# Kernel tuning notes

Measured on AMD Instinct MI355X. Metric: run time of the kernel, lower is better.

The kernel has to match this reference:

```python
import jax, jax.numpy as jnp
import numpy as np
from jax import lax

A = 20            # len(ANCHOR_RATIOS)=4 * len(ANCHOR_SCALES)=5 in neural-motifs config
TGT = 6           # anchor_target_dim
DIM = 512
IN_DIM = 1024
B, H, W = 16, 37, 37


def setup_inputs() -> dict:
    key = jax.random.key(0)
    k1, k2, k3, k4, k5 = jax.random.split(key, 5)
    fmap = jax.random.normal(k1, (B, IN_DIM, H, W), dtype=jnp.float32)
    # conv weights in OIHW, fan-in scaled init
    W1 = jax.random.normal(k2, (DIM, IN_DIM, 3, 3), dtype=jnp.float32) / np.sqrt(IN_DIM * 9)
    b1 = jnp.zeros((DIM,), dtype=jnp.float32)
    W2 = jax.random.normal(k3, (TGT * A, DIM, 1, 1), dtype=jnp.float32) / np.sqrt(DIM)
    b2 = jnp.zeros((TGT * A,), dtype=jnp.float32)
    return {"fmap": fmap, "W1": W1, "b1": b1, "W2": W2, "b2": b2}


def reference(fmap, W1, b1, W2, b2):
    dn = ("NCHW", "OIHW", "NCHW")
    # 3x3 conv, padding=1
    x = lax.conv_general_dilated(fmap, W1, window_strides=(1, 1), padding="SAME",
                                 dimension_numbers=dn) + b1[None, :, None, None]
    # ReLU6
    x = jnp.clip(x, 0.0, 6.0)
    # 1x1 conv -> [B, 6*A, H, W]
    x = lax.conv_general_dilated(x, W2, window_strides=(1, 1), padding="VALID",
                                 dimension_numbers=dn) + b2[None, :, None, None]
    # _reshape_channels: [B, C, H, W] -> [B, H, W, C], then split C -> (A, 6)
    b, c, h, w = x.shape
    x = jnp.transpose(x, (0, 2, 3, 1))
    return x.reshape(b, h, w, A, TGT)
```

## Files before the change

### kernel.cpp

```cpp
#include <hip/hip_runtime.h>
#include <stdint.h>

#define HW   1369
#define QW   39
#define QP   1616
#define QT   1536
#define CIN  1024
#define CMID 512
#define KTOT 9216
#define NTIL 144
#define ASL  12288

typedef float  f32x4  __attribute__((ext_vector_type(4)));
typedef __bf16 bf16x8 __attribute__((ext_vector_type(8)));

__device__ __forceinline__ uint16_t f2bf(float f) {
  uint32_t u = __float_as_uint(f);
  u += 0x7fffu + ((u >> 16) & 1u);
  return (uint16_t)(u >> 16);
}

__device__ __forceinline__ void gll16(const void* g, void* l) {
  const __attribute__((address_space(1))) uint32_t* ga =
      (const __attribute__((address_space(1))) uint32_t*)(uintptr_t)g;
  __attribute__((address_space(3))) uint32_t* la =
      (__attribute__((address_space(3))) uint32_t*)(uint32_t)(uintptr_t)l;
  __builtin_amdgcn_global_load_lds(ga, la, 16, 0, 0);
}

__global__ void k_pad_transpose(const float* __restrict__ fmap, uint16_t* __restrict__ Xp) {
  __shared__ float t[32][33];
  const int b = blockIdx.z;
  const int c0 = blockIdx.y * 32;
  const int p0 = blockIdx.x * 32;
  const int tx = threadIdx.x, ty = threadIdx.y;
  const float* src = fmap + ((size_t)b * CIN + c0) * HW + p0;
#pragma unroll
  for (int i = 0; i < 4; ++i) {
    int cc = ty + i * 8;
    t[cc][tx] = (p0 + tx < HW) ? src[(size_t)cc * HW + tx] : 0.f;
  }
  __syncthreads();
#pragma unroll
  for (int i = 0; i < 4; ++i) {
    int pl = ty + i * 8;
    int p = p0 + pl;
    if (p < HW) {
      int h = p / 37, w = p - h * 37;
      int q = (h + 1) * QW + (w + 1);
      Xp[((size_t)b * QP + q) * CIN + c0 + tx] = f2bf(t[tx][pl]);
    }
  }
}

__global__ void k_pack_bfrag(const float* __restrict__ W1, uint16_t* __restrict__ Bp) {
  const int gid = blockIdx.x * 256 + threadIdx.x;
  const int lane = gid & 63;
  const int f    = gid >> 6;
  const int kk   = f & 1;
  const int o16  = (f >> 1) & 31;
  const int t    = f >> 6;
  const int cb = t / 9, tap = t - cb * 9;
  const int o   = o16 * 16 + (lane & 15);
  const int kap = kk * 32 + (lane >> 4) * 8;
  uint16_t* dst = Bp + (size_t)gid * 8;
#pragma unroll
  for (int e = 0; e < 8; ++e) {
    const int c = cb * 64 + kap + e;
    dst[e] = f2bf(W1[((size_t)o * CIN + c) * 9 + tap]);
  }
}

__global__ void k_pack_w2(const float* __restrict__ W2, uint16_t* __restrict__ W2p) {
  int idx = blockIdx.x * 256 + threadIdx.x;
  int j = idx >> 9, o = idx & 511;
  W2p[idx] = (j < 120) ? f2bf(W2[j * 512 + o]) : (uint16_t)0;
}

__global__ __launch_bounds__(256, 2) void k_conv1(
    const uint16_t* __restrict__ Xp, const uint16_t* __restrict__ Bp,
    const float* __restrict__ b1, uint16_t* __restrict__ x1) {
  __shared__ __align__(16) uint16_t lds[2 * ASL];

  const int tid  = threadIdx.x;
  const int wid  = tid >> 6, lane = tid & 63;
  const int lrow = lane & 15, lq = lane >> 4;
  const int wm   = wid >> 1,  wn = wid & 1;

  const int bid = blockIdx.x;
  const int g   = (bid & 7) * 64 + (bid >> 3);
  const int mt  = g >> 2, nt = g & 3;
  const int batch = mt >> 3, qb = (mt & 7) * 192;
  const int o0 = nt * 128;
  const uint16_t* Xb = Xp + (size_t)batch * QP * CIN;

  const int xorb    = (lrow & 7) << 4;
  const int col_el0 = ((lq * 16) ^ xorb) >> 1;
  const int col_el1 = col_el0 ^ 32;

  const int scol = ((tid & 7) ^ ((tid >> 3) & 7)) * 8;
  const int srow = tid >> 3;

  const uint16_t* Bpl = Bp + (size_t)lane * 8;
  const int o16b = nt * 8 + wn * 4;

  f32x4 acc[6][4] = {};

#define STAGEA(u) do {                                                                \
    if ((u) < NTIL) {                                                                 \
      const int cb_  = (u) / 9;                                                       \
      const int tap_ = (u) - cb_ * 9;                                                 \
      const int off_ = (tap_ / 3) * QW + tap_ % 3;                                    \
      const int c0_  = cb_ << 6;                                                      \
      uint16_t* sa = lds + ((u) & 1) * ASL;                                           \
      _Pragma("unroll")                                                               \
      for (int j = 0; j < 6; ++j)                                                     \
        gll16(Xb + (size_t)(qb + off_ + j * 32 + srow) * CIN + c0_ + scol,            \
              sa + (j * 256 + wid * 64) * 8);                                         \
    }                                                                                 \
  } while (0)

#define LOADB(u, BV) do {                                                             \
    if ((u) < NTIL) {                                                                 \
      _Pragma("unroll")                                                               \
      for (int n = 0; n < 4; ++n)                                                     \
        _Pragma("unroll")                                                             \
        for (int kk = 0; kk < 2; ++kk)                                                \
          BV[n * 2 + kk] = *(const bf16x8*)(                                          \
              Bpl + (((size_t)(u) * 32 + o16b + n) * 2 + kk) * 512);                  \
    }                                                                                 \
  } while (0)

#define TILE(t, BVC, BVN) do {                                                        \
    const uint16_t* As = lds + ((t) & 1) * ASL;                                       \
    asm volatile("s_waitcnt vmcnt(0)" ::: "memory");   \
    asm volatile("s_barrier" ::: "memory");                                           \
    __builtin_amdgcn_sched_barrier(0);                                                \
    STAGEA((t) + 1);                                                                  \
    LOADB((t) + 1, BVN);                                                              \
    bf16x8 av0[6], av1[6];                                                            \
    _Pragma("unroll")                                                                 \
    for (int m = 0; m < 6; ++m) {                                                     \
      const uint16_t* ar = As + (wm * 96 + m * 16 + lrow) * 64;                       \
      av0[m] = *(const bf16x8*)(ar + col_el0);                                        \
      av1[m] = *(const bf16x8*)(ar + col_el1);                                        \
    }                                                                                 \
    __builtin_amdgcn_s_setprio(1);                                                    \
    _Pragma("unroll")                                                                 \
    for (int m = 0; m < 6; ++m)                                                       \
      _Pragma("unroll")                                                               \
      for (int n = 0; n < 4; ++n)                                                     \
        acc[m][n] = __builtin_amdgcn_mfma_f32_16x16x32_bf16(                          \
            av0[m], BVC[n * 2], acc[m][n], 0, 0, 0);                                  \
    _Pragma("unroll")                                                                 \
    for (int m = 0; m < 6; ++m)                                                       \
      _Pragma("unroll")                                                               \
      for (int n = 0; n < 4; ++n)                                                     \
        acc[m][n] = __builtin_amdgcn_mfma_f32_16x16x32_bf16(                          \
            av1[m], BVC[n * 2 + 1], acc[m][n], 0, 0, 0);                              \
    __builtin_amdgcn_s_setprio(0);                                                    \
  } while (0)

  bf16x8 bvX[8], bvY[8];
  LOADB(0, bvX);
  STAGEA(0);

  for (int t = 0; t < NTIL; t += 2) {
    TILE(t,     bvX, bvY);
    TILE(t + 1, bvY, bvX);
  }

  const int qr = lq * 4;
#pragma unroll
  for (int n = 0; n < 4; ++n) {
    const int o = o0 + wn * 64 + n * 16 + lrow;
    const float bias = b1[o];
#pragma unroll
    for (int m = 0; m < 6; ++m) {
#pragma unroll
      for (int v = 0; v < 4; ++v) {
        const int q = qb + wm * 96 + m * 16 + qr + v;
        float x = acc[m][n][v] + bias;
        x = fminf(fmaxf(x, 0.f), 6.f);
        x1[((size_t)batch * QT + q) * CMID + o] = f2bf(x);
      }
    }
  }
#undef TILE
#undef LOADB
#undef STAGEA
}

__global__ __launch_bounds__(256, 2) void k_conv2(
    const uint16_t* __restrict__ x1, const uint16_t* __restrict__ W2p,
    const float* __restrict__ b2, float* __restrict__ out) {
  __shared__ __align__(16) uint16_t lA[128 * 64];
  __shared__ __align__(16) uint16_t lB[128 * 64];
  const int tid = threadIdx.x;
  const int wid = tid >> 6, lane = tid & 63;
  const int b = blockIdx.z, q0 = blockIdx.x * 128;
  const uint16_t* Ab = x1 + (size_t)b * QT * CMID;
  const int wm = wid >> 1, wn = wid & 1;
  const int lrow = lane & 15, lk = (lane >> 4) * 8;
  f32x4 acc[4][4] = {};

  for (int kt = 0; kt < 8; ++kt) {
    const int c0 = kt << 6;
#pragma unroll
    for (int i = 0; i < 4; ++i) {
      int wb = i * 256 + wid * 64;
      int chunk = wb + lane;
      int row = chunk >> 3, ch = chunk & 7;
      gll16(Ab + (size_t)(q0 + row) * CMID + c0 + ch * 8, lA + wb * 8);
      gll16(W2p + (size_t)row * CMID + c0 + ch * 8, lB + wb * 8);
    }
    __syncthreads();
#pragma unroll
    for (int kk = 0; kk < 2; ++kk) {
      bf16x8 av[4], bv[4];
#pragma unroll
      for (int mi = 0; mi < 4; ++mi)
        av[mi] = *(const bf16x8*)(lA + (wm * 64 + mi * 16 + lrow) * 64 + kk * 32 + lk);
#pragma unroll
      for (int ni = 0; ni < 4; ++ni)
        bv[ni] = *(const bf16x8*)(lB + (wn * 64 + ni * 16 + lrow) * 64 + kk * 32 + lk);
#pragma unroll
      for (int mi = 0; mi < 4; ++mi)
#pragma unroll
        for (int ni = 0; ni < 4; ++ni)
          acc[mi][ni] = __builtin_amdgcn_mfma_f32_16x16x32_bf16(av[mi], bv[ni], acc[mi][ni], 0, 0, 0);
    }
    __syncthreads();
  }

  const int qr = (lane >> 4) * 4;
#pragma unroll
  for (int ni = 0; ni < 4; ++ni) {
    int j = wn * 64 + ni * 16 + lrow;
    if (j < 120) {
      float bias = b2[j];
#pragma unroll
      for (int mi = 0; mi < 4; ++mi) {
#pragma unroll
        for (int v = 0; v < 4; ++v) {
          int q = q0 + wm * 64 + mi * 16 + qr + v;
          int h = q / QW, w = q - h * QW;
          if (h < 37 && w < 37) {
            out[((size_t)b * HW + h * 37 + w) * 120 + j] = acc[mi][ni][v] + bias;
          }
        }
      }
    }
  }
}

extern "C" void kernel_launch(void* const* d_in, const int* in_sizes, int n_in,
                              void* d_out, int out_size, void* d_ws, size_t ws_size,
                              hipStream_t stream) {
  const float* fmap = (const float*)d_in[0];
  const float* W1   = (const float*)d_in[1];
  const float* b1   = (const float*)d_in[2];
  const float* W2   = (const float*)d_in[3];
  const float* b2   = (const float*)d_in[4];
  float* out = (float*)d_out;

  uint8_t* ws = (uint8_t*)d_ws;
  const size_t XP_BYTES = (size_t)16 * QP * CIN * 2;
  const size_t BP_BYTES = (size_t)144 * 32 * 2 * 64 * 8 * 2;
  const size_t W2P_BYTES = (size_t)128 * 512 * 2;
  uint16_t* Xp  = (uint16_t*)ws;
  uint16_t* Bp  = (uint16_t*)(ws + XP_BYTES);
  uint16_t* W2p = (uint16_t*)(ws + XP_BYTES + BP_BYTES);
  uint16_t* x1  = (uint16_t*)(ws + XP_BYTES + BP_BYTES + W2P_BYTES);

  hipMemsetAsync(Xp, 0, XP_BYTES, stream);
  k_pad_transpose<<<dim3(43, 32, 16), dim3(32, 8), 0, stream>>>(fmap, Xp);
  k_pack_bfrag<<<dim3(2304), dim3(256), 0, stream>>>(W1, Bp);
  k_pack_w2<<<dim3(256), dim3(256), 0, stream>>>(W2, W2p);
  k_conv1<<<dim3(512), dim3(256), 0, stream>>>(Xp, Bp, b1, x1);
  k_conv2<<<dim3(12, 1, 16), dim3(256), 0, stream>>>(x1, W2p, b2, out);
}
```

Measured before the change: 260.1 us.

## Give each wave a private A slice in conv1 and drop block barriers

The conv1 GEMM is repartitioned so each wave owns 48 output rows across all 128 output channels. Each wave stages its own A rows into a private LDS region, which removes the block-wide s_barrier. B fragments are now fetched with inline-asm global loads split by k-half, and explicit vmcnt waits overlap the next tile's loads with the current MFMAs. The trade-off is that every wave must load all 128 channels of B per tile, roughly doubling B global traffic. It also depends on hand-counted vmcnt values, which can silently break correctness if the number of in-flight loads changes.

```diff
diff --git a/kernel.cpp b/kernel.cpp
--- a/kernel.cpp
+++ b/kernel.cpp
@@ -9,7 +9,6 @@
 #define CMID 512
 #define KTOT 9216
 #define NTIL 144
-#define ASL  12288
 
 typedef float  f32x4  __attribute__((ext_vector_type(4)));
 typedef __bf16 bf16x8 __attribute__((ext_vector_type(8)));
@@ -80,12 +79,11 @@
 __global__ __launch_bounds__(256, 2) void k_conv1(
     const uint16_t* __restrict__ Xp, const uint16_t* __restrict__ Bp,
     const float* __restrict__ b1, uint16_t* __restrict__ x1) {
-  __shared__ __align__(16) uint16_t lds[2 * ASL];
+  __shared__ __align__(16) uint16_t lds[24576];
 
   const int tid  = threadIdx.x;
   const int wid  = tid >> 6, lane = tid & 63;
   const int lrow = lane & 15, lq = lane >> 4;
-  const int wm   = wid >> 1,  wn = wid & 1;
 
   const int bid = blockIdx.x;
   const int g   = (bid & 7) * 64 + (bid >> 3);
@@ -93,18 +91,21 @@
   const int batch = mt >> 3, qb = (mt & 7) * 192;
   const int o0 = nt * 128;
   const uint16_t* Xb = Xp + (size_t)batch * QP * CIN;
+  const int qw = qb + wid * 48;
+
+  const int srow8 = lane >> 3;
+  const int scol  = ((lane & 7) ^ srow8) * 8;
+
+  uint16_t* myl = lds + wid * 6144;
 
   const int xorb    = (lrow & 7) << 4;
   const int col_el0 = ((lq * 16) ^ xorb) >> 1;
   const int col_el1 = col_el0 ^ 32;
 
-  const int scol = ((tid & 7) ^ ((tid >> 3) & 7)) * 8;
-  const int srow = tid >> 3;
-
-  const uint16_t* Bpl = Bp + (size_t)lane * 8;
-  const int o16b = nt * 8 + wn * 4;
-
-  f32x4 acc[6][4] = {};
+  const uint16_t* Bl = Bp + (size_t)lane * 8 + (size_t)nt * 8192;
+
+  f32x4 acc[3][8] = {};
+  bf16x8 bv0[8], bv1[8];
 
 #define STAGEA(u) do {                                                                \
     if ((u) < NTIL) {                                                                 \
@@ -112,74 +113,78 @@
       const int tap_ = (u) - cb_ * 9;                                                 \
       const int off_ = (tap_ / 3) * QW + tap_ % 3;                                    \
       const int c0_  = cb_ << 6;                                                      \
-      uint16_t* sa = lds + ((u) & 1) * ASL;                                           \
+      uint16_t* sl = myl + ((u) & 1) * 3072;                                          \
       _Pragma("unroll")                                                               \
       for (int j = 0; j < 6; ++j)                                                     \
-        gll16(Xb + (size_t)(qb + off_ + j * 32 + srow) * CIN + c0_ + scol,            \
-              sa + (j * 256 + wid * 64) * 8);                                         \
+        gll16(Xb + (size_t)(qw + off_ + j * 8 + srow8) * CIN + c0_ + scol,            \
+              sl + j * 512);                                                          \
     }                                                                                 \
   } while (0)
 
-#define LOADB(u, BV) do {                                                             \
+#define LOADBK(u, kk, BV) do {                                                        \
     if ((u) < NTIL) {                                                                 \
-      _Pragma("unroll")                                                               \
-      for (int n = 0; n < 4; ++n)                                                     \
-        _Pragma("unroll")                                                             \
-        for (int kk = 0; kk < 2; ++kk)                                                \
-          BV[n * 2 + kk] = *(const bf16x8*)(                                          \
-              Bpl + (((size_t)(u) * 32 + o16b + n) * 2 + kk) * 512);                  \
+      const uint16_t* bq = Bl + ((size_t)(u) * 64 + (kk)) * 512;                      \
+      _Pragma("unroll")                                                               \
+      for (int n = 0; n < 8; ++n)                                                     \
+        asm volatile("global_load_dwordx4 %0, %1, off"                                \
+                     : "=v"(BV[n]) : "v"(bq + n * 1024) : "memory");                  \
     }                                                                                 \
   } while (0)
 
-#define TILE(t, BVC, BVN) do {                                                        \
-    const uint16_t* As = lds + ((t) & 1) * ASL;                                       \
-    asm volatile("s_waitcnt vmcnt(0)" ::: "memory");   \
-    asm volatile("s_barrier" ::: "memory");                                           \
+#define TILE(t, W1S, W2S, ISS) do {                                                   \
+    asm volatile(W1S ::: "memory");                          \
     __builtin_amdgcn_sched_barrier(0);                                                \
-    STAGEA((t) + 1);                                                                  \
-    LOADB((t) + 1, BVN);                                                              \
-    bf16x8 av0[6], av1[6];                                                            \
+    const uint16_t* As = myl + ((t) & 1) * 3072;                                      \
+    bf16x8 av0[3], av1[3];                                                            \
     _Pragma("unroll")                                                                 \
-    for (int m = 0; m < 6; ++m) {                                                     \
-      const uint16_t* ar = As + (wm * 96 + m * 16 + lrow) * 64;                       \
+    for (int m = 0; m < 3; ++m) {                                                     \
+      const uint16_t* ar = As + (m * 16 + lrow) * 64;                                 \
       av0[m] = *(const bf16x8*)(ar + col_el0);                                        \
       av1[m] = *(const bf16x8*)(ar + col_el1);                                        \
     }                                                                                 \
     __builtin_amdgcn_s_setprio(1);                                                    \
     _Pragma("unroll")                                                                 \
-    for (int m = 0; m < 6; ++m)                                                       \
-      _Pragma("unroll")                                                               \
-      for (int n = 0; n < 4; ++n)                                                     \
+    for (int m = 0; m < 3; ++m)                                                       \
+      _Pragma("unroll")                                                               \
+      for (int n = 0; n < 8; ++n)                                                     \
         acc[m][n] = __builtin_amdgcn_mfma_f32_16x16x32_bf16(                          \
-            av0[m], BVC[n * 2], acc[m][n], 0, 0, 0);                                  \
+            av0[m], bv0[n], acc[m][n], 0, 0, 0);                                      \
+    __builtin_amdgcn_s_setprio(0);                                                    \
+    if (ISS) { LOADBK((t) + 1, 0, bv0); STAGEA((t) + 1); }                            \
+    asm volatile(W2S ::: "memory");                                 \
+    __builtin_amdgcn_sched_barrier(0);                                                \
+    __builtin_amdgcn_s_setprio(1);                                                    \
     _Pragma("unroll")                                                                 \
-    for (int m = 0; m < 6; ++m)                                                       \
-      _Pragma("unroll")                                                               \
-      for (int n = 0; n < 4; ++n)                                                     \
+    for (int m = 0; m < 3; ++m)                                                       \
+      _Pragma("unroll")                                                               \
+      for (int n = 0; n < 8; ++n)                                                     \
         acc[m][n] = __builtin_amdgcn_mfma_f32_16x16x32_bf16(                          \
-            av1[m], BVC[n * 2 + 1], acc[m][n], 0, 0, 0);                              \
+            av1[m], bv1[n], acc[m][n], 0, 0, 0);                                      \
     __builtin_amdgcn_s_setprio(0);                                                    \
+    if (ISS) LOADBK((t) + 1, 1, bv1);                                                 \
   } while (0)
 
-  bf16x8 bvX[8], bvY[8];
-  LOADB(0, bvX);
+  LOADBK(0, 0, bv0);
   STAGEA(0);
-
-  for (int t = 0; t < NTIL; t += 2) {
-    TILE(t,     bvX, bvY);
-    TILE(t + 1, bvY, bvX);
-  }
+  LOADBK(0, 1, bv1);
+
+  for (int t = 0; t < NTIL - 2; t += 2) {
+    TILE(t,     "s_waitcnt vmcnt(8)",  "s_waitcnt vmcnt(14)", 1);
+    TILE(t + 1, "s_waitcnt vmcnt(8)",  "s_waitcnt vmcnt(14)", 1);
+  }
+  TILE(NTIL - 2, "s_waitcnt vmcnt(8)", "s_waitcnt vmcnt(14)", 1);
+  TILE(NTIL - 1, "s_waitcnt vmcnt(8)", "s_waitcnt vmcnt(0)",  0);
 
   const int qr = lq * 4;
 #pragma unroll
-  for (int n = 0; n < 4; ++n) {
-    const int o = o0 + wn * 64 + n * 16 + lrow;
+  for (int n = 0; n < 8; ++n) {
+    const int o = o0 + n * 16 + lrow;
     const float bias = b1[o];
 #pragma unroll
-    for (int m = 0; m < 6; ++m) {
+    for (int m = 0; m < 3; ++m) {
 #pragma unroll
       for (int v = 0; v < 4; ++v) {
-        const int q = qb + wm * 96 + m * 16 + qr + v;
+        const int q = qw + m * 16 + qr + v;
         float x = acc[m][n][v] + bias;
         x = fminf(fmaxf(x, 0.f), 6.f);
         x1[((size_t)batch * QT + q) * CMID + o] = f2bf(x);
@@ -187,7 +192,7 @@
     }
   }
 #undef TILE
-#undef LOADB
+#undef LOADBK
 #undef STAGEA
 }
 
```

New measurement: 297.5 us. 14.4% more time.

## Stage one halo panel per channel block and reuse it across all nine taps

Applied to the files above, without the earlier changes.

The conv1 implicit GEMM used to stage a separate shifted A tile from global memory for each of the 144 (channel-block, tap) steps. It now loads one 288-row halo panel per 64-channel block into LDS and reads all nine tap offsets from that panel. The swizzle is rebased on the tap row offset so the XOR pattern still matches. This cuts global-to-LDS traffic about ninefold and needs only one barrier per channel block instead of one per tap. In exchange LDS use grows to 72 KB per block, which may limit occupancy at two blocks per CU, and the padded input buffer is enlarged to cover the panel overrun.

```diff
diff --git a/kernel.cpp b/kernel.cpp
--- a/kernel.cpp
+++ b/kernel.cpp
@@ -3,13 +3,12 @@
 
 #define HW   1369
 #define QW   39
-#define QP   1616
+#define QP2  1648
 #define QT   1536
 #define CIN  1024
 #define CMID 512
-#define KTOT 9216
 #define NTIL 144
-#define ASL  12288
+#define PANEL 18432
 
 typedef float  f32x4  __attribute__((ext_vector_type(4)));
 typedef __bf16 bf16x8 __attribute__((ext_vector_type(8)));
@@ -48,7 +47,7 @@
     if (p < HW) {
       int h = p / 37, w = p - h * 37;
       int q = (h + 1) * QW + (w + 1);
-      Xp[((size_t)b * QP + q) * CIN + c0 + tx] = f2bf(t[tx][pl]);
+      Xp[((size_t)b * QP2 + q) * CIN + c0 + tx] = f2bf(t[tx][pl]);
     }
   }
 }
@@ -80,7 +79,7 @@
 __global__ __launch_bounds__(256, 2) void k_conv1(
     const uint16_t* __restrict__ Xp, const uint16_t* __restrict__ Bp,
     const float* __restrict__ b1, uint16_t* __restrict__ x1) {
-  __shared__ __align__(16) uint16_t lds[2 * ASL];
+  __shared__ __align__(16) uint16_t lds[2 * PANEL];
 
   const int tid  = threadIdx.x;
   const int wid  = tid >> 6, lane = tid & 63;
@@ -92,31 +91,23 @@
   const int mt  = g >> 2, nt = g & 3;
   const int batch = mt >> 3, qb = (mt & 7) * 192;
   const int o0 = nt * 128;
-  const uint16_t* Xb = Xp + (size_t)batch * QP * CIN;
-
-  const int xorb    = (lrow & 7) << 4;
-  const int col_el0 = ((lq * 16) ^ xorb) >> 1;
-  const int col_el1 = col_el0 ^ 32;
-
-  const int scol = ((tid & 7) ^ ((tid >> 3) & 7)) * 8;
-  const int srow = tid >> 3;
+  const uint16_t* Xb = Xp + (size_t)batch * QP2 * CIN;
+
+  const int sR8  = lane >> 3;
+  const int sc8  = ((lane & 7) ^ sR8) * 8;
 
   const uint16_t* Bpl = Bp + (size_t)lane * 8;
   const int o16b = nt * 8 + wn * 4;
 
   f32x4 acc[6][4] = {};
-
-#define STAGEA(u) do {                                                                \
-    if ((u) < NTIL) {                                                                 \
-      const int cb_  = (u) / 9;                                                       \
-      const int tap_ = (u) - cb_ * 9;                                                 \
-      const int off_ = (tap_ / 3) * QW + tap_ % 3;                                    \
-      const int c0_  = cb_ << 6;                                                      \
-      uint16_t* sa = lds + ((u) & 1) * ASL;                                           \
-      _Pragma("unroll")                                                               \
-      for (int j = 0; j < 6; ++j)                                                     \
-        gll16(Xb + (size_t)(qb + off_ + j * 32 + srow) * CIN + c0_ + scol,            \
-              sa + (j * 256 + wid * 64) * 8);                                         \
+  bf16x8 bvX[8], bvY[8];
+
+#define STPAN(cb1, call) do {                                                         \
+    if ((cb1) < 16) {                                                                 \
+      const int c0_ = (cb1) << 6;                                                     \
+      const int Rb  = (call) * 32 + wid * 8;                                          \
+      gll16(Xb + (size_t)(qb + Rb + sR8) * CIN + c0_ + sc8,                           \
+            lds + ((cb1) & 1) * PANEL + Rb * 64);                                     \
     }                                                                                 \
   } while (0)
 
@@ -131,20 +122,20 @@
     }                                                                                 \
   } while (0)
 
-#define TILE(t, BVC, BVN) do {                                                        \
-    const uint16_t* As = lds + ((t) & 1) * ASL;                                       \
-    asm volatile("s_waitcnt vmcnt(0)" ::: "memory");   \
-    asm volatile("s_barrier" ::: "memory");                                           \
-    __builtin_amdgcn_sched_barrier(0);                                                \
-    STAGEA((t) + 1);                                                                  \
-    LOADB((t) + 1, BVN);                                                              \
+#define TAP(tap, BVC, BVN) do {                                                       \
+    const int off_ = ((tap) / 3) * QW + (tap) % 3;                                    \
+    const int r7   = (off_ + lrow) & 7;                                               \
+    const int ce0  = ((lq * 16) ^ (r7 << 4)) >> 1;                                    \
+    const int ce1  = ce0 ^ 32;                                                        \
     bf16x8 av0[6], av1[6];                                                            \
     _Pragma("unroll")                                                                 \
     for (int m = 0; m < 6; ++m) {                                                     \
-      const uint16_t* ar = As + (wm * 96 + m * 16 + lrow) * 64;                       \
-      av0[m] = *(const bf16x8*)(ar + col_el0);                                        \
-      av1[m] = *(const bf16x8*)(ar + col_el1);                                        \
+      const uint16_t* ar = pan + (off_ + wm * 96 + m * 16 + lrow) * 64;               \
+      av0[m] = *(const bf16x8*)(ar + ce0);                                            \
+      av1[m] = *(const bf16x8*)(ar + ce1);                                            \
     }                                                                                 \
+    LOADB(cb * 9 + (tap) + 1, BVN);                                                   \
+    STPAN(cb + 1, tap);                                                               \
     __builtin_amdgcn_s_setprio(1);                                                    \
     _Pragma("unroll")                                                                 \
     for (int m = 0; m < 6; ++m)                                                       \
@@ -161,13 +152,23 @@
     __builtin_amdgcn_s_setprio(0);                                                    \
   } while (0)
 
-  bf16x8 bvX[8], bvY[8];
+#define GROUP(CB, B0, B1) do {                                                        \
+    const int cb = (CB);                                                              \
+    asm volatile("s_waitcnt vmcnt(0)" ::: "memory");     \
+    asm volatile("s_barrier" ::: "memory");             \
+    __builtin_amdgcn_sched_barrier(0);                                                \
+    const uint16_t* pan = lds + (cb & 1) * PANEL;                                     \
+    TAP(0, B0, B1); TAP(1, B1, B0); TAP(2, B0, B1);                                   \
+    TAP(3, B1, B0); TAP(4, B0, B1); TAP(5, B1, B0);                                   \
+    TAP(6, B0, B1); TAP(7, B1, B0); TAP(8, B0, B1);                                   \
+  } while (0)
+
+  for (int c = 0; c < 9; ++c) STPAN(0, c);
   LOADB(0, bvX);
-  STAGEA(0);
-
-  for (int t = 0; t < NTIL; t += 2) {
-    TILE(t,     bvX, bvY);
-    TILE(t + 1, bvY, bvX);
+
+  for (int cb2 = 0; cb2 < 16; cb2 += 2) {
+    GROUP(cb2,     bvX, bvY);
+    GROUP(cb2 + 1, bvY, bvX);
   }
 
   const int qr = lq * 4;
@@ -186,9 +187,10 @@
       }
     }
   }
-#undef TILE
+#undef GROUP
+#undef TAP
 #undef LOADB
-#undef STAGEA
+#undef STPAN
 }
 
 __global__ __launch_bounds__(256, 2) void k_conv2(
@@ -265,7 +267,7 @@
   float* out = (float*)d_out;
 
   uint8_t* ws = (uint8_t*)d_ws;
-  const size_t XP_BYTES = (size_t)16 * QP * CIN * 2;
+  const size_t XP_BYTES = (size_t)16 * QP2 * CIN * 2;
   const size_t BP_BYTES = (size_t)144 * 32 * 2 * 64 * 8 * 2;
   const size_t W2P_BYTES = (size_t)128 * 512 * 2;
   uint16_t* Xp  = (uint16_t*)ws;
```

Measured after the change: 336.0 us. 29.2% more time.
